# Kernel tuning notes

Measured on AMD Instinct MI355X. Metric: run time of the kernel, lower is better.

Reference implementation:

```python
import jax, jax.numpy as jnp
from jax import lax
import numpy as np

ITER_ = 10
SMOOTH = 1.0

# ---------- soft skeletonization (clDice-style, 2D) ----------

def _max_pool(x, wh, ww):
    # x: [B,1,H,W]
    return lax.reduce_window(x, -jnp.inf, lax.max, (1, 1, wh, ww), (1, 1, 1, 1), 'SAME')

def _soft_erode(x):
    return jnp.minimum(-_max_pool(-x, 3, 1), -_max_pool(-x, 1, 3))

def _soft_dilate(x):
    return _max_pool(x, 3, 3)

def _soft_open(x):
    return _soft_dilate(_soft_erode(x))

def soft_skel(img, iters):
    skel = jax.nn.relu(img - _soft_open(img))
    for _ in range(iters):
        img = _soft_erode(img)
        delta = jax.nn.relu(img - _soft_open(img))
        skel = skel + jax.nn.relu(delta - skel * delta)
    return skel

# ---------- exact 2D Euclidean distance transform ----------

def _edt2d(mask):
    # mask: [H,W] bool, True = foreground. distance to nearest background pixel.
    H, W = mask.shape
    BIG = jnp.float32(H + W)
    z = ~mask  # background indicator
    def step(d, zr):
        d = jnp.where(zr, 0.0, jnp.minimum(d + 1.0, BIG))
        return d, d
    init = jnp.full((H,), BIG, jnp.float32)
    _, f = lax.scan(step, init, z.T)            # [W,H] forward along rows
    _, b = lax.scan(step, init, z.T[::-1])      # backward
    g = jnp.minimum(f, b[::-1]).T               # [H,W] 1D row distance
    ys = jnp.arange(H, dtype=jnp.float32)
    diff2 = (ys[:, None] - ys[None, :]) ** 2    # [H,H]
    # lower envelope over columns: d2[y,x] = min_y' g[y',x]^2 + (y-y')^2
    d2 = jnp.min(g[None, :, :] ** 2 + diff2[:, :, None], axis=1)  # [H,W]
    return jnp.sqrt(d2)

_edt_batched = jax.vmap(_edt2d)  # [B,H,W] bool -> [B,H,W] float

# ---------- cbDice pieces ----------

def combine_tensors(A, B, C):
    return jnp.where((A != 0) & (B == 0), A * C, B * C)

def get_weights(mask_input, skel_input, prob_flag):
    # mask_input/skel_input: [B,H,W] float
    mask = mask_input > 0.5
    skel = skel_input > 0.5
    dist = lax.stop_gradient(_edt_batched(mask))       # EDT of binary mask, non-diff
    distances = jnp.where(mask, dist, 0.0)
    skel_radius = jnp.where(skel, distances, 0.0)
    rmax = jnp.maximum(jnp.max(skel_radius, axis=(1, 2), keepdims=True), 1.0)
    rmin = jnp.maximum(jnp.min(skel_radius, axis=(1, 2), keepdims=True), 1.0)
    d_clip = jnp.minimum(distances, rmax)
    dist_map_norm = d_clip / rmax
    skel_R_norm = skel_radius / rmax
    I_norm = (rmax - skel_radius + rmin) / rmax        # dim == 2 branch
    I_norm = jnp.where(skel, I_norm, 0.0)
    if prob_flag:
        return dist_map_norm * mask_input, skel_R_norm * mask_input, I_norm * skel_input
    m = mask.astype(jnp.float32)
    s = skel.astype(jnp.float32)
    return dist_map_norm * m, skel_R_norm * m, I_norm * s

def soft_cb_dice_loss(y_pred, y_true):
    p = jax.nn.sigmoid(y_pred)                              # [B,1,H,W]
    pb = jnp.concatenate([1.0 - p, p], axis=1)              # [B,2,H,W]
    pp = jax.nn.softmax(pb, axis=1)[:, 1]                   # [B,H,W]
    yt = jnp.where(y_true > 0, 1.0, 0.0)[:, 0]              # [B,H,W]
    hard = lax.stop_gradient((pp > 0.5).astype(jnp.float32))
    skel_pred_hard = lax.stop_gradient(soft_skel(hard[:, None], ITER_)[:, 0])
    skel_true = lax.stop_gradient(soft_skel(yt[:, None], ITER_)[:, 0])
    skel_pred_prob = skel_pred_hard * pp
    q_vl, q_slvl, q_sl = get_weights(yt, skel_true, False)
    q_vp, q_spvp, q_sp = get_weights(pp, skel_pred_prob, True)
    w_tprec = (jnp.sum(q_sp * q_vl) + SMOOTH) / (jnp.sum(combine_tensors(q_spvp, q_slvl, q_sp)) + SMOOTH)
    w_tsens = (jnp.sum(q_sl * q_vp) + SMOOTH) / (jnp.sum(combine_tensors(q_slvl, q_spvp, q_sl)) + SMOOTH)
    return 1.0 - 2.0 * (w_tprec * w_tsens) / (w_tprec + w_tsens)

def setup_inputs() -> dict:
    key = jax.random.key(0)
    k1, k2 = jax.random.split(key)
    y_pred = jax.random.normal(k1, (4, 1, 256, 256), dtype=jnp.float32)
    y_true = jax.random.randint(k2, (4, 1, 256, 256), 0, 2, dtype=jnp.int32)
    return {"y_pred": y_pred, "y_true": y_true}

def reference(y_pred, y_true):
    return soft_cb_dice_loss(y_pred, y_true)
```

## Files before the change

### kernel.cpp

```cpp
#include <hip/hip_runtime.h>

typedef unsigned long long u64;

#define NIMG 4
#define H 256
#define W 256
#define NPIX (H*W)
#define NTOT (NIMG*NPIX)
#define WPR 4
#define WPI (H*WPR)
#define WPB (NIMG*WPI)
#define XT 16
#define NSKEL 8
#define NEDT 128
#define NB2 (NSKEL+NEDT)

__device__ __forceinline__ void erode_from(const u64 S[][WPR], int y, u64 out[WPR]) {
  u64 c[WPR], up[WPR], dn[WPR];
#pragma unroll
  for (int k = 0; k < WPR; ++k) {
    c[k]  = S[y][k];
    up[k] = (y > 0)     ? S[y-1][k] : ~0ULL;
    dn[k] = (y < H-1)   ? S[y+1][k] : ~0ULL;
  }
#pragma unroll
  for (int k = 0; k < WPR; ++k) {
    u64 l = (c[k] << 1) | ((k > 0)     ? (c[k-1] >> 63) : 1ULL);
    u64 r = (c[k] >> 1) | ((k < WPR-1) ? (c[k+1] << 63) : 0x8000000000000000ULL);
    out[k] = c[k] & up[k] & dn[k] & l & r;
  }
}

__device__ __forceinline__ void dilate_from(const u64 S[][WPR], int y, u64 out[WPR]) {
  u64 v[WPR];
#pragma unroll
  for (int k = 0; k < WPR; ++k) {
    u64 a = S[y][k];
    if (y > 0)   a |= S[y-1][k];
    if (y < H-1) a |= S[y+1][k];
    v[k] = a;
  }
#pragma unroll
  for (int k = 0; k < WPR; ++k) {
    u64 l = (v[k] << 1) | ((k > 0)     ? (v[k-1] >> 63) : 0ULL);
    u64 r = (v[k] >> 1) | ((k < WPR-1) ? (v[k+1] << 63) : 0ULL);
    out[k] = v[k] | l | r;
  }
}

__global__ void __launch_bounds__(256) prep_kernel(
    const float* __restrict__ y_pred, const int* __restrict__ y_true,
    u64* __restrict__ mask_bits, unsigned* __restrict__ rmm_u,
    double* __restrict__ sums, unsigned* __restrict__ cnts) {
  if (blockIdx.x == 0) {
    if (threadIdx.x < 16) rmm_u[threadIdx.x] = (threadIdx.x & 1) ? 0x7F800000u : 0u;
    else if (threadIdx.x < 20) sums[threadIdx.x - 16] = 0.0;
    else if (threadIdx.x < 30) cnts[threadIdx.x - 20] = 0u;
  }
  int i = blockIdx.x * 256 + threadIdx.x;
  float x = y_pred[i];
  float p = 1.0f / (1.0f + expf(-x));
  float q = 1.0f / (1.0f + expf(-(2.0f * p - 1.0f)));
  u64 bt = __ballot(y_true[i] > 0);
  u64 bp = __ballot(q > 0.5f);
  if ((threadIdx.x & 63) == 0) {
    mask_bits[i >> 6] = bt;
    mask_bits[WPB + (i >> 6)] = bp;
  }
}

__global__ void __launch_bounds__(256, 1) morpho_final_kernel(
    const float* __restrict__ y_pred, const int* __restrict__ y_true,
    const u64* __restrict__ mask_bits, u64* __restrict__ skel_bits,
    float* __restrict__ edt, unsigned* __restrict__ rmm_u,
    double* __restrict__ sums, unsigned* __restrict__ cnts,
    float* __restrict__ out) {
  __shared__ u64 SA[H][WPR];
  __shared__ u64 SB[H][WPR];
  __shared__ float col2[H][XT + 1];
  __shared__ u64 srow[H];
  __shared__ float smax[4], smin[4];
  __shared__ float part[4][4];
  int t = threadIdx.x;

  if (blockIdx.x < NSKEL) {
    int bi = blockIdx.x;
    int y = t;
    int base = bi * WPI;
    u64 a[WPR], cur[WPR], e[WPR], d[WPR], sk[WPR];
#pragma unroll
    for (int k = 0; k < WPR; ++k) { a[k] = mask_bits[base + y*WPR + k]; SA[y][k] = a[k]; }
    __syncthreads();
    erode_from(SA, y, e);
#pragma unroll
    for (int k = 0; k < WPR; ++k) SB[y][k] = e[k];
    __syncthreads();
    dilate_from(SB, y, d);
#pragma unroll
    for (int k = 0; k < WPR; ++k) { sk[k] = a[k] & ~d[k]; cur[k] = e[k]; }
    u64 (*P)[WPR] = SB;
    u64 (*Q)[WPR] = SA;
    for (int it = 0; it < 10; ++it) {
      erode_from(P, y, e);
#pragma unroll
      for (int k = 0; k < WPR; ++k) Q[y][k] = e[k];
      __syncthreads();
      dilate_from(Q, y, d);
#pragma unroll
      for (int k = 0; k < WPR; ++k) { sk[k] |= cur[k] & ~d[k]; cur[k] = e[k]; }
      u64 (*T)[WPR] = P; P = Q; Q = T;
    }
#pragma unroll
    for (int k = 0; k < WPR; ++k) skel_bits[base + y*WPR + k] = sk[k];
    __syncthreads();
    if (t == 0) {
      __threadfence();
      atomicAdd(&cnts[bi], 1u);
      atomicAdd(&cnts[9], 1u);
    }
    return;
  }

  {
    int bt = blockIdx.x - NSKEL;
    int bi = bt >> 4;
    int xt = bt & 15;
    int x0 = xt * XT;
    int kx = x0 >> 6;
    int sh0 = x0 & 63;
    {
      int y = t;
      const u64* row = mask_bits + bi*WPI + y*WPR;
      u64 z[WPR];
#pragma unroll
      for (int k = 0; k < WPR; ++k) z[k] = ~row[k];
#pragma unroll
      for (int xx = 0; xx < XT; ++xx) {
        int x = x0 + xx;
        int bx = x & 63;
        int ld = 512;
        {
          u64 w = z[kx] & ((bx == 63) ? ~0ULL : ((1ULL << (bx+1)) - 1ULL));
          for (int k = kx; ; ) {
            if (w) { int pos = 63 - __builtin_clzll(w) + (k << 6); ld = x - pos; break; }
            if (--k < 0) break;
            w = z[k];
          }
        }
        int rd = 512;
        {
          u64 w = z[kx] & (~0ULL << bx);
          for (int k = kx; ; ) {
            if (w) { int pos = __builtin_ctzll(w) + (k << 6); rd = pos - x; break; }
            if (++k > WPR-1) break;
            w = z[k];
          }
        }
        int g = min(ld, rd);
        col2[y][xx] = (float)(g * g);
      }
    }
    __syncthreads();
    int x  = t & (XT - 1);
    int yg = t >> 4;
    float dist_r[16];
#pragma unroll
    for (int j = 0; j < 16; ++j) {
      int y = yg * 16 + j;
      float best = col2[y][x];
      for (int k = 1; k < H; ++k) {
        float k2 = (float)(k * k);
        if (k2 >= best) break;
        int ym = y - k, yq = y + k;
        if (ym >= 0) best = fminf(best, col2[ym][x] + k2);
        if (yq < H)  best = fminf(best, col2[yq][x] + k2);
      }
      float dist = sqrtf(best);
      dist_r[j] = dist;
      edt[bi*NPIX + y*W + x0 + x] = dist;
    }
    if (t == 0) {
      while (__hip_atomic_load(&cnts[bi], __ATOMIC_RELAXED,
                               __HIP_MEMORY_SCOPE_AGENT) == 0u)
        __builtin_amdgcn_s_sleep(2);
    }
    __syncthreads();
    srow[t] = __hip_atomic_load(&skel_bits[bi*WPI + t*WPR + kx],
                                __ATOMIC_RELAXED, __HIP_MEMORY_SCOPE_AGENT);
    __syncthreads();
    float vmax = 0.0f, vmin = 3.0e38f;
#pragma unroll
    for (int j = 0; j < 16; ++j) {
      int y = yg * 16 + j;
      u64 sw = srow[y];
      int sb = (int)((sw >> (sh0 + x)) & 1ULL);
      float srad = sb ? dist_r[j] : 0.0f;
      vmax = fmaxf(vmax, srad);
      vmin = fminf(vmin, srad);
    }
    for (int o = 32; o > 0; o >>= 1) {
      vmax = fmaxf(vmax, __shfl_down(vmax, o, 64));
      vmin = fminf(vmin, __shfl_down(vmin, o, 64));
    }
    int wave = t >> 6, lane = t & 63;
    if (lane == 0) { smax[wave] = vmax; smin[wave] = vmin; }
    __syncthreads();
    if (t == 0) {
      float mx = smax[0], mn = smin[0];
      for (int wv = 1; wv < 4; ++wv) { mx = fmaxf(mx, smax[wv]); mn = fminf(mn, smin[wv]); }
      atomicMax(&rmm_u[bi*2 + 0], __float_as_uint(mx));
      atomicMin(&rmm_u[bi*2 + 1], __float_as_uint(mn));
      __threadfence();
      atomicAdd(&cnts[9], 1u);
      while (__hip_atomic_load(&cnts[9], __ATOMIC_RELAXED,
                               __HIP_MEMORY_SCOPE_AGENT) < NB2)
        __builtin_amdgcn_s_sleep(2);
    }
    __syncthreads();
    __threadfence();
  }

  {
    int fb = blockIdx.x - NSKEL;
    int i0 = (fb * 256 + t) * 8;
    int img = i0 >> 16;
    int wi  = i0 >> 6;
    int b0  = i0 & 63;
    u64 mw_t = mask_bits[wi];
    u64 sw_t = skel_bits[wi];
    u64 sw_p = skel_bits[WPB + wi];
    float4 xp0 = *(const float4*)(y_pred + i0);
    float4 xp1 = *(const float4*)(y_pred + i0 + 4);
    float4 dt0 = *(const float4*)(edt + i0);
    float4 dt1 = *(const float4*)(edt + i0 + 4);
    float4 dp0 = *(const float4*)(edt + NTOT + i0);
    float4 dp1 = *(const float4*)(edt + NTOT + i0 + 4);
    float rmax_t = fmaxf(__uint_as_float(rmm_u[img*2 + 0]), 1.0f);
    float rmin_t = fmaxf(__uint_as_float(rmm_u[img*2 + 1]), 1.0f);
    float rmax_p = fmaxf(__uint_as_float(rmm_u[(4+img)*2 + 0]), 1.0f);
    float rmin_p = fmaxf(__uint_as_float(rmm_u[(4+img)*2 + 1]), 1.0f);
    float xs[8] = {xp0.x,xp0.y,xp0.z,xp0.w,xp1.x,xp1.y,xp1.z,xp1.w};
    float dts[8] = {dt0.x,dt0.y,dt0.z,dt0.w,dt1.x,dt1.y,dt1.z,dt1.w};
    float dps[8] = {dp0.x,dp0.y,dp0.z,dp0.w,dp1.x,dp1.y,dp1.z,dp1.w};
    float q1 = 0.f, q2 = 0.f, q3 = 0.f, q4 = 0.f;
#pragma unroll
    for (int j = 0; j < 8; ++j) {
      int b = b0 + j;
      float p = 1.0f / (1.0f + expf(-xs[j]));
      float ppv = 1.0f / (1.0f + expf(-(2.0f * p - 1.0f)));
      int m_t = (int)((mw_t >> b) & 1ULL);
      int s_t = (int)((sw_t >> b) & 1ULL);
      float distances_t = m_t ? dts[j] : 0.0f;
      float skelrad_t   = s_t ? distances_t : 0.0f;
      float dmn_t = fminf(distances_t, rmax_t) / rmax_t;
      float srn_t = skelrad_t / rmax_t;
      float In_t  = s_t ? (rmax_t - skelrad_t + rmin_t) / rmax_t : 0.0f;
      float q_vl   = m_t ? dmn_t : 0.0f;
      float q_slvl = m_t ? srn_t : 0.0f;
      float q_sl   = s_t ? In_t  : 0.0f;
      int s_pb = (int)((sw_p >> b) & 1ULL);
      float skel_in_p = s_pb ? ppv : 0.0f;
      bool msk_p = ppv > 0.5f;
      bool sk_p  = skel_in_p > 0.5f;
      float distances_p = msk_p ? dps[j] : 0.0f;
      float skelrad_p   = sk_p ? distances_p : 0.0f;
      float dmn_p = fminf(distances_p, rmax_p) / rmax_p;
      float srn_p = skelrad_p / rmax_p;
      float In_p  = sk_p ? (rmax_p - skelrad_p + rmin_p) / rmax_p : 0.0f;
      float q_vp   = dmn_p * ppv;
      float q_spvp = srn_p * ppv;
      float q_sp   = In_p * skel_in_p;
      q1 += q_sp * q_vl;
      q2 += (q_spvp != 0.0f && q_slvl == 0.0f) ? q_spvp * q_sp : q_slvl * q_sp;
      q3 += q_sl * q_vp;
      q4 += (q_slvl != 0.0f && q_spvp == 0.0f) ? q_slvl * q_sl : q_spvp * q_sl;
    }
    for (int o = 32; o > 0; o >>= 1) {
      q1 += __shfl_down(q1, o, 64);
      q2 += __shfl_down(q2, o, 64);
      q3 += __shfl_down(q3, o, 64);
      q4 += __shfl_down(q4, o, 64);
    }
    int wave = t >> 6, lane = t & 63;
    if (lane == 0) { part[wave][0]=q1; part[wave][1]=q2; part[wave][2]=q3; part[wave][3]=q4; }
    __syncthreads();
    if (t == 0) {
      float a0=0,a1=0,a2=0,a3=0;
      for (int wv = 0; wv < 4; ++wv) {
        a0 += part[wv][0]; a1 += part[wv][1]; a2 += part[wv][2]; a3 += part[wv][3];
      }
      atomicAdd(&sums[0], (double)a0);
      atomicAdd(&sums[1], (double)a1);
      atomicAdd(&sums[2], (double)a2);
      atomicAdd(&sums[3], (double)a3);
      __threadfence();
      unsigned c = atomicAdd(&cnts[8], 1u);
      if (c == NEDT - 1) {
        double s0 = atomicAdd(&sums[0], 0.0);
        double s1 = atomicAdd(&sums[1], 0.0);
        double s2 = atomicAdd(&sums[2], 0.0);
        double s3 = atomicAdd(&sums[3], 0.0);
        double wp  = (s0 + 1.0) / (s1 + 1.0);
        double wsn = (s2 + 1.0) / (s3 + 1.0);
        out[0] = (float)(1.0 - 2.0 * (wp * wsn) / (wp + wsn));
      }
    }
  }
}

extern "C" void kernel_launch(void* const* d_in, const int* in_sizes, int n_in,
                              void* d_out, int out_size, void* d_ws, size_t ws_size,
                              hipStream_t stream) {
  (void)in_sizes; (void)n_in; (void)out_size; (void)ws_size;
  const float* y_pred = (const float*)d_in[0];
  const int*   y_true = (const int*)d_in[1];
  float* out = (float*)d_out;
  char* ws = (char*)d_ws;

  float* edt       = (float*)(ws + 0);
  u64*   mask_bits = (u64*)  (ws + 2097152);
  u64*   skel_bits = (u64*)  (ws + 2162688);
  unsigned* rmm_u  = (unsigned*)(ws + 2228224);
  double* sums     = (double*)(ws + 2228288);
  unsigned* cnts   = (unsigned*)(ws + 2228320);

  prep_kernel<<<NTOT/256, 256, 0, stream>>>(y_pred, y_true, mask_bits, rmm_u, sums, cnts);
  morpho_final_kernel<<<NB2, 256, 0, stream>>>(y_pred, y_true, mask_bits, skel_bits,
                                               edt, rmm_u, sums, cnts, out);
}
```

Baseline: 94.40 us.

## Keep EDT in registers, pair true/pred EDT per tile, sync per image

Each EDT block now computes both the target and prediction distance transforms for one narrower column tile of a single image. The distances stay in registers for the final weighted-sum phase, so the global edt buffer and its write-back and re-read go away. The grid-wide barrier is replaced by a per-image counter barrier across the 32 tiles of that image. In exchange each block does two EDT passes serially with narrower tiles, which means more redundant row scans, and the per-image spin-waits remain.

```diff
diff --git a/kernel.cpp b/kernel.cpp
--- a/kernel.cpp
+++ b/kernel.cpp
@@ -10,10 +10,10 @@
 #define WPR 4
 #define WPI (H*WPR)
 #define WPB (NIMG*WPI)
-#define XT 16
+#define XT 8
 #define NSKEL 8
-#define NEDT 128
-#define NB2 (NSKEL+NEDT)
+#define NTILE 128
+#define NB2 (NSKEL+NTILE)
 
 __device__ __forceinline__ void erode_from(const u64 S[][WPR], int y, u64 out[WPR]) {
   u64 c[WPR], up[WPR], dn[WPR];
@@ -55,7 +55,7 @@
   if (blockIdx.x == 0) {
     if (threadIdx.x < 16) rmm_u[threadIdx.x] = (threadIdx.x & 1) ? 0x7F800000u : 0u;
     else if (threadIdx.x < 20) sums[threadIdx.x - 16] = 0.0;
-    else if (threadIdx.x < 30) cnts[threadIdx.x - 20] = 0u;
+    else if (threadIdx.x < 34) cnts[threadIdx.x - 20] = 0u;
   }
   int i = blockIdx.x * 256 + threadIdx.x;
   float x = y_pred[i];
@@ -69,18 +69,69 @@
   }
 }
 
-__global__ void __launch_bounds__(256, 1) morpho_final_kernel(
-    const float* __restrict__ y_pred, const int* __restrict__ y_true,
-    const u64* __restrict__ mask_bits, u64* __restrict__ skel_bits,
-    float* __restrict__ edt, unsigned* __restrict__ rmm_u,
+#define EDT_PASS(MROW, DIST, SAVE_MASK)                                        \
+  {                                                                            \
+    int y = t;                                                                 \
+    const u64* row = (MROW) + y*WPR;                                           \
+    u64 z[WPR];                                                                \
+    _Pragma("unroll")                                                          \
+    for (int k = 0; k < WPR; ++k) z[k] = ~row[k];         \
+    if (SAVE_MASK) msk_row[y] = row[kx];                                       \
+    _Pragma("unroll")                                                          \
+    for (int xx = 0; xx < XT; ++xx) {                                          \
+      int x = x0 + xx;                                                         \
+      int bx = x & 63;                                                         \
+      int ld = 512;                                                            \
+      {                                                                        \
+        u64 w = z[kx] & ((bx == 63) ? ~0ULL : ((1ULL << (bx+1)) - 1ULL));      \
+        for (int k = kx; ; ) {                                                 \
+          if (w) { int pos = 63 - __builtin_clzll(w) + (k << 6); ld = x - pos; break; } \
+          if (--k < 0) break;                                                  \
+          w = z[k];                                                            \
+        }                                                                      \
+      }                                                                        \
+      int rd = 512;                                                            \
+      {                                                                        \
+        u64 w = z[kx] & (~0ULL << bx);                                         \
+        for (int k = kx; ; ) {                                                 \
+          if (w) { int pos = __builtin_ctzll(w) + (k << 6); rd = pos - x; break; } \
+          if (++k > WPR-1) break;                                              \
+          w = z[k];                                                            \
+        }                                                                      \
+      }                                                                        \
+      int g = min(ld, rd);                                                     \
+      col2[y][xx] = (float)(g * g);                                            \
+    }                                                                          \
+  }                                                                            \
+  __syncthreads();                                                             \
+  _Pragma("unroll")                                                            \
+  for (int j = 0; j < 8; ++j) {                                                \
+    int y = yg * 8 + j;                                                        \
+    float best = col2[y][xq];                                                  \
+    for (int k = 1; k < H; ++k) {                                              \
+      float k2 = (float)(k * k);                                               \
+      if (k2 >= best) break;                \
+      int ym = y - k, yd = y + k;                                              \
+      if (ym >= 0) best = fminf(best, col2[ym][xq] + k2);                      \
+      if (yd < H)  best = fminf(best, col2[yd][xq] + k2);                      \
+    }                                                                          \
+    (DIST)[j] = sqrtf(best);                                                   \
+  }                                                                            \
+  __syncthreads();
+
+__global__ void __launch_bounds__(256, 1) fused_kernel(
+    const float* __restrict__ y_pred, const u64* __restrict__ mask_bits,
+    u64* __restrict__ skel_bits, unsigned* __restrict__ rmm_u,
     double* __restrict__ sums, unsigned* __restrict__ cnts,
     float* __restrict__ out) {
   __shared__ u64 SA[H][WPR];
   __shared__ u64 SB[H][WPR];
   __shared__ float col2[H][XT + 1];
-  __shared__ u64 srow[H];
-  __shared__ float smax[4], smin[4];
-  __shared__ float part[4][4];
+  __shared__ u64 srow_t[H];
+  __shared__ u64 srow_p[H];
+  __shared__ u64 msk_row[H];
+  __shared__ float redf[4][4];
+  __shared__ unsigned smm[4];
   int t = threadIdx.x;
 
   if (blockIdx.x < NSKEL) {
@@ -116,194 +167,149 @@
     if (t == 0) {
       __threadfence();
       atomicAdd(&cnts[bi], 1u);
-      atomicAdd(&cnts[9], 1u);
     }
     return;
   }
 
-  {
-    int bt = blockIdx.x - NSKEL;
-    int bi = bt >> 4;
-    int xt = bt & 15;
-    int x0 = xt * XT;
-    int kx = x0 >> 6;
-    int sh0 = x0 & 63;
-    {
-      int y = t;
-      const u64* row = mask_bits + bi*WPI + y*WPR;
-      u64 z[WPR];
-#pragma unroll
-      for (int k = 0; k < WPR; ++k) z[k] = ~row[k];
-#pragma unroll
-      for (int xx = 0; xx < XT; ++xx) {
-        int x = x0 + xx;
-        int bx = x & 63;
-        int ld = 512;
-        {
-          u64 w = z[kx] & ((bx == 63) ? ~0ULL : ((1ULL << (bx+1)) - 1ULL));
-          for (int k = kx; ; ) {
-            if (w) { int pos = 63 - __builtin_clzll(w) + (k << 6); ld = x - pos; break; }
-            if (--k < 0) break;
-            w = z[k];
-          }
-        }
-        int rd = 512;
-        {
-          u64 w = z[kx] & (~0ULL << bx);
-          for (int k = kx; ; ) {
-            if (w) { int pos = __builtin_ctzll(w) + (k << 6); rd = pos - x; break; }
-            if (++k > WPR-1) break;
-            w = z[k];
-          }
-        }
-        int g = min(ld, rd);
-        col2[y][xx] = (float)(g * g);
-      }
-    }
-    __syncthreads();
-    int x  = t & (XT - 1);
-    int yg = t >> 4;
-    float dist_r[16];
-#pragma unroll
-    for (int j = 0; j < 16; ++j) {
-      int y = yg * 16 + j;
-      float best = col2[y][x];
-      for (int k = 1; k < H; ++k) {
-        float k2 = (float)(k * k);
-        if (k2 >= best) break;
-        int ym = y - k, yq = y + k;
-        if (ym >= 0) best = fminf(best, col2[ym][x] + k2);
-        if (yq < H)  best = fminf(best, col2[yq][x] + k2);
-      }
-      float dist = sqrtf(best);
-      dist_r[j] = dist;
-      edt[bi*NPIX + y*W + x0 + x] = dist;
-    }
-    if (t == 0) {
-      while (__hip_atomic_load(&cnts[bi], __ATOMIC_RELAXED,
-                               __HIP_MEMORY_SCOPE_AGENT) == 0u)
-        __builtin_amdgcn_s_sleep(2);
-    }
-    __syncthreads();
-    srow[t] = __hip_atomic_load(&skel_bits[bi*WPI + t*WPR + kx],
+  int tb  = blockIdx.x - NSKEL;
+  int img = tb >> 5;
+  int xt  = tb & 31;
+  int x0  = xt * XT;
+  int kx  = x0 >> 6;
+  int sh0 = x0 & 63;
+  int xq  = t & (XT - 1);
+  int yg  = t >> 3;
+
+  float dist_t[8], dist_p[8];
+  EDT_PASS(mask_bits + img*WPI,       dist_t, 1)
+  EDT_PASS(mask_bits + (4+img)*WPI,   dist_p, 0)
+
+  if (t == 0) {
+    while (__hip_atomic_load(&cnts[img], __ATOMIC_RELAXED,
+                             __HIP_MEMORY_SCOPE_AGENT) == 0u)
+      __builtin_amdgcn_s_sleep(2);
+    while (__hip_atomic_load(&cnts[4+img], __ATOMIC_RELAXED,
+                             __HIP_MEMORY_SCOPE_AGENT) == 0u)
+      __builtin_amdgcn_s_sleep(2);
+  }
+  __syncthreads();
+  srow_t[t] = __hip_atomic_load(&skel_bits[img*WPI + t*WPR + kx],
                                 __ATOMIC_RELAXED, __HIP_MEMORY_SCOPE_AGENT);
-    __syncthreads();
-    float vmax = 0.0f, vmin = 3.0e38f;
-#pragma unroll
-    for (int j = 0; j < 16; ++j) {
-      int y = yg * 16 + j;
-      u64 sw = srow[y];
-      int sb = (int)((sw >> (sh0 + x)) & 1ULL);
-      float srad = sb ? dist_r[j] : 0.0f;
-      vmax = fmaxf(vmax, srad);
-      vmin = fminf(vmin, srad);
-    }
-    for (int o = 32; o > 0; o >>= 1) {
-      vmax = fmaxf(vmax, __shfl_down(vmax, o, 64));
-      vmin = fminf(vmin, __shfl_down(vmin, o, 64));
-    }
-    int wave = t >> 6, lane = t & 63;
-    if (lane == 0) { smax[wave] = vmax; smin[wave] = vmin; }
-    __syncthreads();
-    if (t == 0) {
-      float mx = smax[0], mn = smin[0];
-      for (int wv = 1; wv < 4; ++wv) { mx = fmaxf(mx, smax[wv]); mn = fminf(mn, smin[wv]); }
-      atomicMax(&rmm_u[bi*2 + 0], __float_as_uint(mx));
-      atomicMin(&rmm_u[bi*2 + 1], __float_as_uint(mn));
-      __threadfence();
-      atomicAdd(&cnts[9], 1u);
-      while (__hip_atomic_load(&cnts[9], __ATOMIC_RELAXED,
-                               __HIP_MEMORY_SCOPE_AGENT) < NB2)
-        __builtin_amdgcn_s_sleep(2);
-    }
-    __syncthreads();
+  srow_p[t] = __hip_atomic_load(&skel_bits[(4+img)*WPI + t*WPR + kx],
+                                __ATOMIC_RELAXED, __HIP_MEMORY_SCOPE_AGENT);
+  __syncthreads();
+
+  float vmax_t = 0.0f, vmin_t = 3.0e38f, vmax_p = 0.0f, vmin_p = 3.0e38f;
+#pragma unroll
+  for (int j = 0; j < 8; ++j) {
+    int y = yg * 8 + j;
+    int sb_t = (int)((srow_t[y] >> (sh0 + xq)) & 1ULL);
+    int sb_p = (int)((srow_p[y] >> (sh0 + xq)) & 1ULL);
+    float srt = sb_t ? dist_t[j] : 0.0f;
+    float srp = sb_p ? dist_p[j] : 0.0f;
+    vmax_t = fmaxf(vmax_t, srt); vmin_t = fminf(vmin_t, srt);
+    vmax_p = fmaxf(vmax_p, srp); vmin_p = fminf(vmin_p, srp);
+  }
+  for (int o = 32; o > 0; o >>= 1) {
+    vmax_t = fmaxf(vmax_t, __shfl_down(vmax_t, o, 64));
+    vmin_t = fminf(vmin_t, __shfl_down(vmin_t, o, 64));
+    vmax_p = fmaxf(vmax_p, __shfl_down(vmax_p, o, 64));
+    vmin_p = fminf(vmin_p, __shfl_down(vmin_p, o, 64));
+  }
+  int wave = t >> 6, lane = t & 63;
+  if (lane == 0) { redf[wave][0]=vmax_t; redf[wave][1]=vmin_t;
+                   redf[wave][2]=vmax_p; redf[wave][3]=vmin_p; }
+  __syncthreads();
+  if (t == 0) {
+    float mxt=redf[0][0], mnt=redf[0][1], mxp=redf[0][2], mnp=redf[0][3];
+    for (int wv = 1; wv < 4; ++wv) {
+      mxt = fmaxf(mxt, redf[wv][0]); mnt = fminf(mnt, redf[wv][1]);
+      mxp = fmaxf(mxp, redf[wv][2]); mnp = fminf(mnp, redf[wv][3]);
+    }
+    atomicMax(&rmm_u[img*2 + 0], __float_as_uint(mxt));
+    atomicMin(&rmm_u[img*2 + 1], __float_as_uint(mnt));
+    atomicMax(&rmm_u[(4+img)*2 + 0], __float_as_uint(mxp));
+    atomicMin(&rmm_u[(4+img)*2 + 1], __float_as_uint(mnp));
+    __hip_atomic_fetch_add(&cnts[10+img], 1u, __ATOMIC_RELEASE,
+                           __HIP_MEMORY_SCOPE_AGENT);
+    while (__hip_atomic_load(&cnts[10+img], __ATOMIC_RELAXED,
+                             __HIP_MEMORY_SCOPE_AGENT) < 32u)
+      __builtin_amdgcn_s_sleep(2);
+  }
+  __syncthreads();
+  if (t < 4) {
+    int idx = (t < 2) ? (img*2 + t) : ((4+img)*2 + (t-2));
+    smm[t] = __hip_atomic_load(&rmm_u[idx], __ATOMIC_RELAXED,
+                               __HIP_MEMORY_SCOPE_AGENT);
+  }
+  __syncthreads();
+  float rmax_t = fmaxf(__uint_as_float(smm[0]), 1.0f);
+  float rmin_t = fmaxf(__uint_as_float(smm[1]), 1.0f);
+  float rmax_p = fmaxf(__uint_as_float(smm[2]), 1.0f);
+  float rmin_p = fmaxf(__uint_as_float(smm[3]), 1.0f);
+
+  float q1 = 0.f, q2 = 0.f, q3 = 0.f, q4 = 0.f;
+#pragma unroll
+  for (int j = 0; j < 8; ++j) {
+    int y = yg * 8 + j;
+    float xv = y_pred[img*NPIX + y*W + x0 + xq];
+    float p = 1.0f / (1.0f + expf(-xv));
+    float ppv = 1.0f / (1.0f + expf(-(2.0f * p - 1.0f)));
+    int b = sh0 + xq;
+    int m_t  = (int)((msk_row[y] >> b) & 1ULL);
+    int s_t  = (int)((srow_t[y] >> b) & 1ULL);
+    int s_pb = (int)((srow_p[y] >> b) & 1ULL);
+    float distances_t = m_t ? dist_t[j] : 0.0f;
+    float skelrad_t   = s_t ? distances_t : 0.0f;
+    float dmn_t = fminf(distances_t, rmax_t) / rmax_t;
+    float srn_t = skelrad_t / rmax_t;
+    float In_t  = s_t ? (rmax_t - skelrad_t + rmin_t) / rmax_t : 0.0f;
+    float q_vl   = m_t ? dmn_t : 0.0f;
+    float q_slvl = m_t ? srn_t : 0.0f;
+    float q_sl   = s_t ? In_t  : 0.0f;
+    float skel_in_p = s_pb ? ppv : 0.0f;
+    bool msk_p = ppv > 0.5f;
+    bool sk_p  = skel_in_p > 0.5f;
+    float distances_p = msk_p ? dist_p[j] : 0.0f;
+    float skelrad_p   = sk_p ? distances_p : 0.0f;
+    float dmn_p = fminf(distances_p, rmax_p) / rmax_p;
+    float srn_p = skelrad_p / rmax_p;
+    float In_p  = sk_p ? (rmax_p - skelrad_p + rmin_p) / rmax_p : 0.0f;
+    float q_vp   = dmn_p * ppv;
+    float q_spvp = srn_p * ppv;
+    float q_sp   = In_p * skel_in_p;
+    q1 += q_sp * q_vl;
+    q2 += (q_spvp != 0.0f && q_slvl == 0.0f) ? q_spvp * q_sp : q_slvl * q_sp;
+    q3 += q_sl * q_vp;
+    q4 += (q_slvl != 0.0f && q_spvp == 0.0f) ? q_slvl * q_sl : q_spvp * q_sl;
+  }
+  for (int o = 32; o > 0; o >>= 1) {
+    q1 += __shfl_down(q1, o, 64);
+    q2 += __shfl_down(q2, o, 64);
+    q3 += __shfl_down(q3, o, 64);
+    q4 += __shfl_down(q4, o, 64);
+  }
+  if (lane == 0) { redf[wave][0]=q1; redf[wave][1]=q2; redf[wave][2]=q3; redf[wave][3]=q4; }
+  __syncthreads();
+  if (t == 0) {
+    float a0=0,a1=0,a2=0,a3=0;
+    for (int wv = 0; wv < 4; ++wv) {
+      a0 += redf[wv][0]; a1 += redf[wv][1]; a2 += redf[wv][2]; a3 += redf[wv][3];
+    }
+    atomicAdd(&sums[0], (double)a0);
+    atomicAdd(&sums[1], (double)a1);
+    atomicAdd(&sums[2], (double)a2);
+    atomicAdd(&sums[3], (double)a3);
     __threadfence();
-  }
-
-  {
-    int fb = blockIdx.x - NSKEL;
-    int i0 = (fb * 256 + t) * 8;
-    int img = i0 >> 16;
-    int wi  = i0 >> 6;
-    int b0  = i0 & 63;
-    u64 mw_t = mask_bits[wi];
-    u64 sw_t = skel_bits[wi];
-    u64 sw_p = skel_bits[WPB + wi];
-    float4 xp0 = *(const float4*)(y_pred + i0);
-    float4 xp1 = *(const float4*)(y_pred + i0 + 4);
-    float4 dt0 = *(const float4*)(edt + i0);
-    float4 dt1 = *(const float4*)(edt + i0 + 4);
-    float4 dp0 = *(const float4*)(edt + NTOT + i0);
-    float4 dp1 = *(const float4*)(edt + NTOT + i0 + 4);
-    float rmax_t = fmaxf(__uint_as_float(rmm_u[img*2 + 0]), 1.0f);
-    float rmin_t = fmaxf(__uint_as_float(rmm_u[img*2 + 1]), 1.0f);
-    float rmax_p = fmaxf(__uint_as_float(rmm_u[(4+img)*2 + 0]), 1.0f);
-    float rmin_p = fmaxf(__uint_as_float(rmm_u[(4+img)*2 + 1]), 1.0f);
-    float xs[8] = {xp0.x,xp0.y,xp0.z,xp0.w,xp1.x,xp1.y,xp1.z,xp1.w};
-    float dts[8] = {dt0.x,dt0.y,dt0.z,dt0.w,dt1.x,dt1.y,dt1.z,dt1.w};
-    float dps[8] = {dp0.x,dp0.y,dp0.z,dp0.w,dp1.x,dp1.y,dp1.z,dp1.w};
-    float q1 = 0.f, q2 = 0.f, q3 = 0.f, q4 = 0.f;
-#pragma unroll
-    for (int j = 0; j < 8; ++j) {
-      int b = b0 + j;
-      float p = 1.0f / (1.0f + expf(-xs[j]));
-      float ppv = 1.0f / (1.0f + expf(-(2.0f * p - 1.0f)));
-      int m_t = (int)((mw_t >> b) & 1ULL);
-      int s_t = (int)((sw_t >> b) & 1ULL);
-      float distances_t = m_t ? dts[j] : 0.0f;
-      float skelrad_t   = s_t ? distances_t : 0.0f;
-      float dmn_t = fminf(distances_t, rmax_t) / rmax_t;
-      float srn_t = skelrad_t / rmax_t;
-      float In_t  = s_t ? (rmax_t - skelrad_t + rmin_t) / rmax_t : 0.0f;
-      float q_vl   = m_t ? dmn_t : 0.0f;
-      float q_slvl = m_t ? srn_t : 0.0f;
-      float q_sl   = s_t ? In_t  : 0.0f;
-      int s_pb = (int)((sw_p >> b) & 1ULL);
-      float skel_in_p = s_pb ? ppv : 0.0f;
-      bool msk_p = ppv > 0.5f;
-      bool sk_p  = skel_in_p > 0.5f;
-      float distances_p = msk_p ? dps[j] : 0.0f;
-      float skelrad_p   = sk_p ? distances_p : 0.0f;
-      float dmn_p = fminf(distances_p, rmax_p) / rmax_p;
-      float srn_p = skelrad_p / rmax_p;
-      float In_p  = sk_p ? (rmax_p - skelrad_p + rmin_p) / rmax_p : 0.0f;
-      float q_vp   = dmn_p * ppv;
-      float q_spvp = srn_p * ppv;
-      float q_sp   = In_p * skel_in_p;
-      q1 += q_sp * q_vl;
-      q2 += (q_spvp != 0.0f && q_slvl == 0.0f) ? q_spvp * q_sp : q_slvl * q_sp;
-      q3 += q_sl * q_vp;
-      q4 += (q_slvl != 0.0f && q_spvp == 0.0f) ? q_slvl * q_sl : q_spvp * q_sl;
-    }
-    for (int o = 32; o > 0; o >>= 1) {
-      q1 += __shfl_down(q1, o, 64);
-      q2 += __shfl_down(q2, o, 64);
-      q3 += __shfl_down(q3, o, 64);
-      q4 += __shfl_down(q4, o, 64);
-    }
-    int wave = t >> 6, lane = t & 63;
-    if (lane == 0) { part[wave][0]=q1; part[wave][1]=q2; part[wave][2]=q3; part[wave][3]=q4; }
-    __syncthreads();
-    if (t == 0) {
-      float a0=0,a1=0,a2=0,a3=0;
-      for (int wv = 0; wv < 4; ++wv) {
-        a0 += part[wv][0]; a1 += part[wv][1]; a2 += part[wv][2]; a3 += part[wv][3];
-      }
-      atomicAdd(&sums[0], (double)a0);
-      atomicAdd(&sums[1], (double)a1);
-      atomicAdd(&sums[2], (double)a2);
-      atomicAdd(&sums[3], (double)a3);
-      __threadfence();
-      unsigned c = atomicAdd(&cnts[8], 1u);
-      if (c == NEDT - 1) {
-        double s0 = atomicAdd(&sums[0], 0.0);
-        double s1 = atomicAdd(&sums[1], 0.0);
-        double s2 = atomicAdd(&sums[2], 0.0);
-        double s3 = atomicAdd(&sums[3], 0.0);
-        double wp  = (s0 + 1.0) / (s1 + 1.0);
-        double wsn = (s2 + 1.0) / (s3 + 1.0);
-        out[0] = (float)(1.0 - 2.0 * (wp * wsn) / (wp + wsn));
-      }
+    unsigned c = atomicAdd(&cnts[8], 1u);
+    if (c == NTILE - 1) {
+      double s0 = atomicAdd(&sums[0], 0.0);
+      double s1 = atomicAdd(&sums[1], 0.0);
+      double s2 = atomicAdd(&sums[2], 0.0);
+      double s3 = atomicAdd(&sums[3], 0.0);
+      double wp  = (s0 + 1.0) / (s1 + 1.0);
+      double wsn = (s2 + 1.0) / (s3 + 1.0);
+      out[0] = (float)(1.0 - 2.0 * (wp * wsn) / (wp + wsn));
     }
   }
 }
@@ -317,14 +323,12 @@
   float* out = (float*)d_out;
   char* ws = (char*)d_ws;
 
-  float* edt       = (float*)(ws + 0);
-  u64*   mask_bits = (u64*)  (ws + 2097152);
-  u64*   skel_bits = (u64*)  (ws + 2162688);
-  unsigned* rmm_u  = (unsigned*)(ws + 2228224);
-  double* sums     = (double*)(ws + 2228288);
-  unsigned* cnts   = (unsigned*)(ws + 2228320);
+  u64*   mask_bits = (u64*)  (ws + 0);
+  u64*   skel_bits = (u64*)  (ws + 65536);
+  unsigned* rmm_u  = (unsigned*)(ws + 131072);
+  double* sums     = (double*)(ws + 131136);
+  unsigned* cnts   = (unsigned*)(ws + 131168);
 
   prep_kernel<<<NTOT/256, 256, 0, stream>>>(y_pred, y_true, mask_bits, rmm_u, sums, cnts);
-  morpho_final_kernel<<<NB2, 256, 0, stream>>>(y_pred, y_true, mask_bits, skel_bits,
-                                               edt, rmm_u, sums, cnts, out);
-}
+  fused_kernel<<<NB2, 256, 0, stream>>>(y_pred, mask_bits, skel_bits, rmm_u, sums, cnts, out);
+}
```

Result: faster. 90.99 us (-3.6%).
